# Kernel tuning notes

Hardware: AMD Instinct MI355X
Metric: run time of the kernel (lower is better)

The kernel has to match this reference:

```python
import jax, jax.numpy as jnp
import numpy as np

TEMPERATURE = 2.0


def _safe_l2(diff):
    # l2 norm over last axis, safe at zero (diagonal) so it matches norm(2,-1) forward
    s = jnp.sum(diff * diff, axis=-1)
    return jnp.sqrt(jnp.where(s > 0, s, 1.0)) * (s > 0)


def _offdiag_cols(n):
    # column indices of off-diagonal elements per row, matching
    # masked_select((1-eye).bool()).view(n, n-1) row-major ordering
    k = jnp.arange(n - 1)[None, :]          # [1, n-1]
    i = jnp.arange(n)[:, None]              # [n, 1]
    return k + (k >= i)                     # [n, n-1]


def setup_inputs() -> dict:
    key = jax.random.key(0)
    kf, kl = jax.random.split(key)
    features = jax.random.normal(kf, (512, 128), dtype=jnp.float32)
    labels = jax.random.normal(kl, (256, 2), dtype=jnp.float32)
    return {"features": features, "labels": labels}


def reference(features, labels):
    labels2 = jnp.concatenate([labels, labels], axis=0)  # labels.repeat(2,1)
    # label diff: l1 pairwise  [n, n]
    label_diffs = jnp.abs(labels2[:, None, :] - labels2[None, :, :]).sum(-1)
    # feature sim: negative l2 pairwise, divided by temperature  [n, n]
    logits = -_safe_l2(features[:, None, :] - features[None, :, :]) / TEMPERATURE
    n = logits.shape[0]

    rows = jnp.arange(n)[:, None]
    cols = _offdiag_cols(n)
    logits_od = logits[rows, cols]            # [n, n-1]
    ld_od = label_diffs[rows, cols]           # [n, n-1]

    logits_max = jax.lax.stop_gradient(jnp.max(logits_od, axis=1, keepdims=True))
    logits_od = logits_od - logits_max
    exp_logits = jnp.exp(logits_od)           # [n, n-1]

    # neg_mask[i, k, j] = label_diffs[i, j] >= label_diffs[i, k]
    neg_mask = ld_od[:, None, :] >= ld_od[:, :, None]          # [n, n-1, n-1] bool
    denom = jnp.einsum('ikj,ij->ik', neg_mask.astype(exp_logits.dtype), exp_logits)
    log_probs = logits_od - jnp.log(denom)    # [n, n-1]
    loss = -jnp.sum(log_probs) / (n * (n - 1))
    return loss
```

## Files before the change

kernel.cpp:

```cpp
#include <hip/hip_runtime.h>
#include <math.h>

#define N 512
#define C 256
#define D 128

__global__ __launch_bounds__(256) void k1_logits(const float* __restrict__ feat,
                                                 float* __restrict__ lg) {
    const int tid = threadIdx.x;
    const int row0 = (blockIdx.x >> 4) << 5;
    const int col0 = (blockIdx.x & 15) << 5;

    __shared__ float4 As[32][32];
    __shared__ float4 Bs[32][32];

    const float4* f4 = (const float4*)feat;
    {
        const int r = tid >> 5, c4 = tid & 31;
#pragma unroll
        for (int p = 0; p < 4; ++p) {
            const int rr = r + p * 8;
            const int sc = c4 ^ ((rr >> 1) & 7);
            As[rr][sc] = f4[(size_t)(row0 + rr) * 32 + c4];
            Bs[rr][sc] = f4[(size_t)(col0 + rr) * 32 + c4];
        }
    }
    __syncthreads();

    const int ty = tid >> 4, tx = tid & 15;
    const int r0 = 2 * ty, r1 = 2 * ty + 1;
    const int c0 = 2 * tx, c1 = 2 * tx + 1;
    const int sa = ty & 7, sb = tx & 7;

    float s00 = 0.f, s01 = 0.f, s10 = 0.f, s11 = 0.f;
#pragma unroll 8
    for (int q = 0; q < 32; ++q) {
        float4 a0 = As[r0][q ^ sa];
        float4 a1 = As[r1][q ^ sa];
        float4 b0 = Bs[c0][q ^ sb];
        float4 b1 = Bs[c1][q ^ sb];
        float t;
        t = a0.x - b0.x; s00 = fmaf(t, t, s00);
        t = a0.y - b0.y; s00 = fmaf(t, t, s00);
        t = a0.z - b0.z; s00 = fmaf(t, t, s00);
        t = a0.w - b0.w; s00 = fmaf(t, t, s00);
        t = a0.x - b1.x; s01 = fmaf(t, t, s01);
        t = a0.y - b1.y; s01 = fmaf(t, t, s01);
        t = a0.z - b1.z; s01 = fmaf(t, t, s01);
        t = a0.w - b1.w; s01 = fmaf(t, t, s01);
        t = a1.x - b0.x; s10 = fmaf(t, t, s10);
        t = a1.y - b0.y; s10 = fmaf(t, t, s10);
        t = a1.z - b0.z; s10 = fmaf(t, t, s10);
        t = a1.w - b0.w; s10 = fmaf(t, t, s10);
        t = a1.x - b1.x; s11 = fmaf(t, t, s11);
        t = a1.y - b1.y; s11 = fmaf(t, t, s11);
        t = a1.z - b1.z; s11 = fmaf(t, t, s11);
        t = a1.w - b1.w; s11 = fmaf(t, t, s11);
    }
    float l00 = (s00 > 0.f) ? -0.5f * sqrtf(s00) : 0.f;
    float l01 = (s01 > 0.f) ? -0.5f * sqrtf(s01) : 0.f;
    float l10 = (s10 > 0.f) ? -0.5f * sqrtf(s10) : 0.f;
    float l11 = (s11 > 0.f) ? -0.5f * sqrtf(s11) : 0.f;

    *(float2*)(lg + (size_t)(row0 + r0) * N + col0 + c0) = make_float2(l00, l01);
    *(float2*)(lg + (size_t)(row0 + r1) * N + col0 + c0) = make_float2(l10, l11);
}

__global__ __launch_bounds__(256) void k2_row(const float* __restrict__ lg,
                                              const float* __restrict__ labels,
                                              float* __restrict__ ld2,
                                              float* __restrict__ evs,
                                              float* __restrict__ rowsum) {
    const int i = blockIdx.x;
    const int c = threadIdx.x;

    const float la = lg[(size_t)i * N + c];
    const float lb = lg[(size_t)i * N + c + 256];

    float m = -1e30f;
    if (c != i) m = la;
    if (c + 256 != i) m = fmaxf(m, lb);
    __shared__ float redm[4];
#pragma unroll
    for (int off = 32; off > 0; off >>= 1) m = fmaxf(m, __shfl_xor(m, off, 64));
    if ((c & 63) == 0) redm[c >> 6] = m;
    __syncthreads();
    m = fmaxf(fmaxf(redm[0], redm[1]), fmaxf(redm[2], redm[3]));

    float ea = (c == i) ? 0.f : __expf(la - m);
    float eb = (c + 256 == i) ? 0.f : __expf(lb - m);
    evs[(size_t)i * C + c] = ea + eb;

    const float2 lc = ((const float2*)labels)[c];
    const float2 li = ((const float2*)labels)[i & 255];
    ld2[(size_t)i * C + c] = fabsf(li.x - lc.x) + fabsf(li.y - lc.y);

    float s = la + lb;
    __shared__ float reds[4];
#pragma unroll
    for (int off = 32; off > 0; off >>= 1) s += __shfl_xor(s, off, 64);
    if ((c & 63) == 0) reds[c >> 6] = s;
    __syncthreads();
    if (c == 0) rowsum[i] = (reds[0] + reds[1] + reds[2] + reds[3]) - 511.f * m;
}

__global__ __launch_bounds__(256) void k3_den(const float* __restrict__ ld2,
                                              const float* __restrict__ evs,
                                              const float* __restrict__ rowsum,
                                              float* __restrict__ rowout) {
    const int i = blockIdx.x;
    const int c = threadIdx.x;
    const float* __restrict__ rl = ld2 + (size_t)i * C;
    const float* __restrict__ re = evs + (size_t)i * C;
    const float ldk = rl[c];

    float d0 = 0.f, d1 = 0.f, d2 = 0.f, d3 = 0.f;
#pragma unroll 8
    for (int q = 0; q < C; q += 4) {
        float a0 = rl[q + 0], a1 = rl[q + 1], a2 = rl[q + 2], a3 = rl[q + 3];
        float b0 = re[q + 0], b1 = re[q + 1], b2 = re[q + 2], b3 = re[q + 3];
        d0 += (a0 >= ldk) ? b0 : 0.f;
        d1 += (a1 >= ldk) ? b1 : 0.f;
        d2 += (a2 >= ldk) ? b2 : 0.f;
        d3 += (a3 >= ldk) ? b3 : 0.f;
    }
    const float lden = __logf((d0 + d1) + (d2 + d3));

    __shared__ float red[4];
    __shared__ float lci;
    if (c == (i & 255)) lci = lden;
    float s = lden;
#pragma unroll
    for (int off = 32; off > 0; off >>= 1) s += __shfl_xor(s, off, 64);
    if ((c & 63) == 0) red[c >> 6] = s;
    __syncthreads();
    if (c == 0) {
        float tot = red[0] + red[1] + red[2] + red[3];
        rowout[i] = rowsum[i] - (2.f * tot - lci);
    }
}

__global__ __launch_bounds__(256) void k4_reduce(const float* __restrict__ rowout,
                                                 float* __restrict__ out) {
    const int tid = threadIdx.x;
    double s = 0.0;
    for (int j = tid; j < N; j += 256) s += (double)rowout[j];
#pragma unroll
    for (int off = 32; off > 0; off >>= 1) s += __shfl_down(s, off, 64);
    __shared__ double sd[4];
    if ((tid & 63) == 0) sd[tid >> 6] = s;
    __syncthreads();
    if (tid == 0) {
        double t = sd[0] + sd[1] + sd[2] + sd[3];
        out[0] = (float)(-t / ((double)N * (double)(N - 1)));
    }
}

extern "C" void kernel_launch(void* const* d_in, const int* in_sizes, int n_in,
                              void* d_out, int out_size, void* d_ws, size_t ws_size,
                              hipStream_t stream) {
    const float* feat   = (const float*)d_in[0];
    const float* labels = (const float*)d_in[1];
    float* out = (float*)d_out;

    float* lg     = (float*)d_ws;
    float* ld2    = lg + (size_t)N * N;
    float* evs    = ld2 + (size_t)N * C;
    float* rowsum = evs + (size_t)N * C;
    float* rowout = rowsum + N;

    k1_logits<<<256, 256, 0, stream>>>(feat, lg);
    k2_row  <<<N,   256, 0, stream>>>(lg, labels, ld2, evs, rowsum);
    k3_den  <<<N,   256, 0, stream>>>(ld2, evs, rowsum, rowout);
    k4_reduce<<<1,  256, 0, stream>>>(rowout, out);
}
```

Baseline: 20.62 us.

## Fuse row softmax, denominator and final reduction into one kernel with atomics

Merges the per-row exp/label-diff kernel with the denominator kernel by keeping the label diffs and exp values in shared memory instead of writing them to global memory. It also replaces the final single-block reduction kernel with a double-precision atomic accumulation plus a last-block-done counter. The accumulator is reset in the first kernel. This cuts two kernel launches and the global round trips for the intermediates. In exchange it adds atomic contention on one address and a summation order that is no longer deterministic.

```diff
diff --git a/kernel.cpp b/kernel.cpp
--- a/kernel.cpp
+++ b/kernel.cpp
@@ -5,9 +5,13 @@
 #define C 256
 #define D 128
 
-__global__ __launch_bounds__(256) void k1_logits(const float* __restrict__ feat,
-                                                 float* __restrict__ lg) {
+__global__ __launch_bounds__(256) void ka_logits(const float* __restrict__ feat,
+                                                 float* __restrict__ lg,
+                                                 double* __restrict__ acc,
+                                                 unsigned* __restrict__ cnt) {
     const int tid = threadIdx.x;
+    if (blockIdx.x == 0 && tid == 0) { *acc = 0.0; *cnt = 0u; }
+
     const int row0 = (blockIdx.x >> 4) << 5;
     const int col0 = (blockIdx.x & 15) << 5;
 
@@ -66,13 +70,18 @@
     *(float2*)(lg + (size_t)(row0 + r1) * N + col0 + c0) = make_float2(l10, l11);
 }
 
-__global__ __launch_bounds__(256) void k2_row(const float* __restrict__ lg,
+__global__ __launch_bounds__(256) void kb_row(const float* __restrict__ lg,
                                               const float* __restrict__ labels,
-                                              float* __restrict__ ld2,
-                                              float* __restrict__ evs,
-                                              float* __restrict__ rowsum) {
+                                              double* __restrict__ acc,
+                                              unsigned* __restrict__ cnt,
+                                              float* __restrict__ out) {
     const int i = blockIdx.x;
     const int c = threadIdx.x;
+
+    __shared__ alignas(16) float sld[C];
+    __shared__ alignas(16) float sev[C];
+    __shared__ float redm[4], reds[4], redl[4];
+    __shared__ float lci;
 
     const float la = lg[(size_t)i * N + c];
     const float lb = lg[(size_t)i * N + c + 256];
@@ -80,79 +89,58 @@
     float m = -1e30f;
     if (c != i) m = la;
     if (c + 256 != i) m = fmaxf(m, lb);
-    __shared__ float redm[4];
 #pragma unroll
     for (int off = 32; off > 0; off >>= 1) m = fmaxf(m, __shfl_xor(m, off, 64));
     if ((c & 63) == 0) redm[c >> 6] = m;
     __syncthreads();
     m = fmaxf(fmaxf(redm[0], redm[1]), fmaxf(redm[2], redm[3]));
 
-    float ea = (c == i) ? 0.f : __expf(la - m);
-    float eb = (c + 256 == i) ? 0.f : __expf(lb - m);
-    evs[(size_t)i * C + c] = ea + eb;
+    const float ea = (c == i) ? 0.f : __expf(la - m);
+    const float eb = (c + 256 == i) ? 0.f : __expf(lb - m);
+    sev[c] = ea + eb;
 
-    const float2 lc = ((const float2*)labels)[c];
-    const float2 li = ((const float2*)labels)[i & 255];
-    ld2[(size_t)i * C + c] = fabsf(li.x - lc.x) + fabsf(li.y - lc.y);
+    const float2 lc2 = ((const float2*)labels)[c];
+    const float2 li2 = ((const float2*)labels)[i & 255];
+    const float ldk = fabsf(li2.x - lc2.x) + fabsf(li2.y - lc2.y);
+    sld[c] = ldk;
 
     float s = la + lb;
-    __shared__ float reds[4];
 #pragma unroll
     for (int off = 32; off > 0; off >>= 1) s += __shfl_xor(s, off, 64);
     if ((c & 63) == 0) reds[c >> 6] = s;
     __syncthreads();
-    if (c == 0) rowsum[i] = (reds[0] + reds[1] + reds[2] + reds[3]) - 511.f * m;
-}
+    const float rowsum = (reds[0] + reds[1] + reds[2] + reds[3]) - 511.f * m;
 
-__global__ __launch_bounds__(256) void k3_den(const float* __restrict__ ld2,
-                                              const float* __restrict__ evs,
-                                              const float* __restrict__ rowsum,
-                                              float* __restrict__ rowout) {
-    const int i = blockIdx.x;
-    const int c = threadIdx.x;
-    const float* __restrict__ rl = ld2 + (size_t)i * C;
-    const float* __restrict__ re = evs + (size_t)i * C;
-    const float ldk = rl[c];
-
+    const float4* a4 = (const float4*)sld;
+    const float4* b4 = (const float4*)sev;
     float d0 = 0.f, d1 = 0.f, d2 = 0.f, d3 = 0.f;
 #pragma unroll 8
-    for (int q = 0; q < C; q += 4) {
-        float a0 = rl[q + 0], a1 = rl[q + 1], a2 = rl[q + 2], a3 = rl[q + 3];
-        float b0 = re[q + 0], b1 = re[q + 1], b2 = re[q + 2], b3 = re[q + 3];
-        d0 += (a0 >= ldk) ? b0 : 0.f;
-        d1 += (a1 >= ldk) ? b1 : 0.f;
-        d2 += (a2 >= ldk) ? b2 : 0.f;
-        d3 += (a3 >= ldk) ? b3 : 0.f;
+    for (int q = 0; q < C / 4; ++q) {
+        float4 a = a4[q];
+        float4 b = b4[q];
+        d0 += (a.x >= ldk) ? b.x : 0.f;
+        d1 += (a.y >= ldk) ? b.y : 0.f;
+        d2 += (a.z >= ldk) ? b.z : 0.f;
+        d3 += (a.w >= ldk) ? b.w : 0.f;
     }
     const float lden = __logf((d0 + d1) + (d2 + d3));
 
-    __shared__ float red[4];
-    __shared__ float lci;
     if (c == (i & 255)) lci = lden;
-    float s = lden;
+    float t = lden;
 #pragma unroll
-    for (int off = 32; off > 0; off >>= 1) s += __shfl_xor(s, off, 64);
-    if ((c & 63) == 0) red[c >> 6] = s;
+    for (int off = 32; off > 0; off >>= 1) t += __shfl_xor(t, off, 64);
+    if ((c & 63) == 0) redl[c >> 6] = t;
     __syncthreads();
     if (c == 0) {
-        float tot = red[0] + red[1] + red[2] + red[3];
-        rowout[i] = rowsum[i] - (2.f * tot - lci);
-    }
-}
-
-__global__ __launch_bounds__(256) void k4_reduce(const float* __restrict__ rowout,
-                                                 float* __restrict__ out) {
-    const int tid = threadIdx.x;
-    double s = 0.0;
-    for (int j = tid; j < N; j += 256) s += (double)rowout[j];
-#pragma unroll
-    for (int off = 32; off > 0; off >>= 1) s += __shfl_down(s, off, 64);
-    __shared__ double sd[4];
-    if ((tid & 63) == 0) sd[tid >> 6] = s;
-    __syncthreads();
-    if (tid == 0) {
-        double t = sd[0] + sd[1] + sd[2] + sd[3];
-        out[0] = (float)(-t / ((double)N * (double)(N - 1)));
+        const float tot = redl[0] + redl[1] + redl[2] + redl[3];
+        const float part = rowsum - (2.f * tot - lci);
+        atomicAdd(acc, (double)part);
+        __threadfence();
+        const unsigned prev = atomicAdd(cnt, 1u);
+        if (prev == (unsigned)(N - 1)) {
+            const double total = atomicAdd(acc, 0.0);
+            out[0] = (float)(-total / ((double)N * (double)(N - 1)));
+        }
     }
 }
 
@@ -163,14 +151,10 @@
     const float* labels = (const float*)d_in[1];
     float* out = (float*)d_out;
 
-    float* lg     = (float*)d_ws;
-    float* ld2    = lg + (size_t)N * N;
-    float* evs    = ld2 + (size_t)N * C;
-    float* rowsum = evs + (size_t)N * C;
-    float* rowout = rowsum + N;
+    float*    lg  = (float*)d_ws;
+    double*   acc = (double*)((char*)d_ws + (size_t)N * N * sizeof(float));
+    unsigned* cnt = (unsigned*)(acc + 1);
 
-    k1_logits<<<256, 256, 0, stream>>>(feat, lg);
-    k2_row  <<<N,   256, 0, stream>>>(lg, labels, ld2, evs, rowsum);
-    k3_den  <<<N,   256, 0, stream>>>(ld2, evs, rowsum, rowout);
-    k4_reduce<<<1,  256, 0, stream>>>(rowout, out);
+    ka_logits<<<256, 256, 0, stream>>>(feat, lg, acc, cnt);
+    kb_row  <<<N,   256, 0, stream>>>(lg, labels, acc, cnt, out);
 }
```

Measured after the change: 27.02 us. +31.0%, slower.

## Fuse row softmax and denominator kernels, move label diffs into logits kernel

Applied to the files above, without the earlier changes.

Merges the per-row exp/max kernel with the denominator kernel so the exp values stay in shared memory instead of going through a global scratch buffer. The label L1 difference table moves into the first kernel, with each block writing two rows. This removes one kernel launch plus the global write and read of the exp and rowsum arrays. The cost is extra label work in the logits kernel and one more barrier in the fused row kernel.

```diff
diff --git a/kernel.cpp b/kernel.cpp
--- a/kernel.cpp
+++ b/kernel.cpp
@@ -6,8 +6,23 @@
 #define D 128
 
 __global__ __launch_bounds__(256) void k1_logits(const float* __restrict__ feat,
-                                                 float* __restrict__ lg) {
+                                                 const float* __restrict__ labels,
+                                                 float* __restrict__ lg,
+                                                 float* __restrict__ ld2) {
     const int tid = threadIdx.x;
+
+    {
+        const int i0 = blockIdx.x << 1;
+#pragma unroll
+        for (int e = tid; e < 2 * C; e += 256) {
+            const int row = i0 + (e >> 8);
+            const int cc  = e & 255;
+            const float2 lc2 = ((const float2*)labels)[cc];
+            const float2 li2 = ((const float2*)labels)[row & 255];
+            ld2[(size_t)row * C + cc] = fabsf(li2.x - lc2.x) + fabsf(li2.y - lc2.y);
+        }
+    }
+
     const int row0 = (blockIdx.x >> 4) << 5;
     const int col0 = (blockIdx.x & 15) << 5;
 
@@ -66,13 +81,15 @@
     *(float2*)(lg + (size_t)(row0 + r1) * N + col0 + c0) = make_float2(l10, l11);
 }
 
-__global__ __launch_bounds__(256) void k2_row(const float* __restrict__ lg,
-                                              const float* __restrict__ labels,
-                                              float* __restrict__ ld2,
-                                              float* __restrict__ evs,
-                                              float* __restrict__ rowsum) {
+__global__ __launch_bounds__(256) void k23_row(const float* __restrict__ lg,
+                                               const float* __restrict__ ld2,
+                                               float* __restrict__ rowout) {
     const int i = blockIdx.x;
     const int c = threadIdx.x;
+
+    __shared__ alignas(16) float sev[C];
+    __shared__ float redm[4], reds[4], redl[4];
+    __shared__ float lci;
 
     const float la = lg[(size_t)i * N + c];
     const float lb = lg[(size_t)i * N + c + 256];
@@ -80,63 +97,48 @@
     float m = -1e30f;
     if (c != i) m = la;
     if (c + 256 != i) m = fmaxf(m, lb);
-    __shared__ float redm[4];
 #pragma unroll
     for (int off = 32; off > 0; off >>= 1) m = fmaxf(m, __shfl_xor(m, off, 64));
     if ((c & 63) == 0) redm[c >> 6] = m;
     __syncthreads();
     m = fmaxf(fmaxf(redm[0], redm[1]), fmaxf(redm[2], redm[3]));
 
-    float ea = (c == i) ? 0.f : __expf(la - m);
-    float eb = (c + 256 == i) ? 0.f : __expf(lb - m);
-    evs[(size_t)i * C + c] = ea + eb;
-
-    const float2 lc = ((const float2*)labels)[c];
-    const float2 li = ((const float2*)labels)[i & 255];
-    ld2[(size_t)i * C + c] = fabsf(li.x - lc.x) + fabsf(li.y - lc.y);
+    const float ea = (c == i) ? 0.f : __expf(la - m);
+    const float eb = (c + 256 == i) ? 0.f : __expf(lb - m);
+    sev[c] = ea + eb;
 
     float s = la + lb;
-    __shared__ float reds[4];
 #pragma unroll
     for (int off = 32; off > 0; off >>= 1) s += __shfl_xor(s, off, 64);
     if ((c & 63) == 0) reds[c >> 6] = s;
     __syncthreads();
-    if (c == 0) rowsum[i] = (reds[0] + reds[1] + reds[2] + reds[3]) - 511.f * m;
-}
+    const float rowsum = (reds[0] + reds[1] + reds[2] + reds[3]) - 511.f * m;
 
-__global__ __launch_bounds__(256) void k3_den(const float* __restrict__ ld2,
-                                              const float* __restrict__ evs,
-                                              const float* __restrict__ rowsum,
-                                              float* __restrict__ rowout) {
-    const int i = blockIdx.x;
-    const int c = threadIdx.x;
     const float* __restrict__ rl = ld2 + (size_t)i * C;
-    const float* __restrict__ re = evs + (size_t)i * C;
     const float ldk = rl[c];
-
+    const float4* e4 = (const float4*)sev;
     float d0 = 0.f, d1 = 0.f, d2 = 0.f, d3 = 0.f;
 #pragma unroll 8
-    for (int q = 0; q < C; q += 4) {
-        float a0 = rl[q + 0], a1 = rl[q + 1], a2 = rl[q + 2], a3 = rl[q + 3];
-        float b0 = re[q + 0], b1 = re[q + 1], b2 = re[q + 2], b3 = re[q + 3];
-        d0 += (a0 >= ldk) ? b0 : 0.f;
-        d1 += (a1 >= ldk) ? b1 : 0.f;
-        d2 += (a2 >= ldk) ? b2 : 0.f;
-        d3 += (a3 >= ldk) ? b3 : 0.f;
+    for (int q = 0; q < C / 4; ++q) {
+        const float a0 = rl[4 * q + 0], a1 = rl[4 * q + 1];
+        const float a2 = rl[4 * q + 2], a3 = rl[4 * q + 3];
+        const float4 ev = e4[q];
+        d0 += (a0 >= ldk) ? ev.x : 0.f;
+        d1 += (a1 >= ldk) ? ev.y : 0.f;
+        d2 += (a2 >= ldk) ? ev.z : 0.f;
+        d3 += (a3 >= ldk) ? ev.w : 0.f;
     }
     const float lden = __logf((d0 + d1) + (d2 + d3));
 
-    __shared__ float red[4];
-    __shared__ float lci;
     if (c == (i & 255)) lci = lden;
-    float s = lden;
+    float t = lden;
 #pragma unroll
-    for (int off = 32; off > 0; off >>= 1) s += __shfl_xor(s, off, 64);
-    if ((c & 63) == 0) red[c >> 6] = s;
+    for (int off = 32; off > 0; off >>= 1) t += __shfl_xor(t, off, 64);
+    if ((c & 63) == 0) redl[c >> 6] = t;
     __syncthreads();
     if (c == 0) {
-        float tot = red[0] + red[1] + red[2] + red[3];
-        rowout[i] = rowsum[i] - (2.f * tot - lci);
+        const float tot = redl[0] + redl[1] + redl[2] + redl[3];
+        rowout[i] = rowsum - (2.f * tot - lci);
     }
 }
 
@@ -165,12 +167,9 @@
 
     float* lg     = (float*)d_ws;
     float* ld2    = lg + (size_t)N * N;
-    float* evs    = ld2 + (size_t)N * C;
-    float* rowsum = evs + (size_t)N * C;
-    float* rowout = rowsum + N;
+    float* rowout = ld2 + (size_t)N * C;
 
-    k1_logits<<<256, 256, 0, stream>>>(feat, lg);
-    k2_row  <<<N,   256, 0, stream>>>(lg, labels, ld2, evs, rowsum);
-    k3_den  <<<N,   256, 0, stream>>>(ld2, evs, rowsum, rowout);
+    k1_logits<<<256, 256, 0, stream>>>(feat, labels, lg, ld2);
+    k23_row <<<N,   256, 0, stream>>>(lg, ld2, rowout);
     k4_reduce<<<1,  256, 0, stream>>>(rowout, out);
 }
```

After: 18.90 us, median of 2. 1.09x faster.
